# Optimization experiments

Hardware: AMD Instinct MI355X
Metric: run time of the kernel (lower is better)

## Reference

```python
import math
import jax, jax.numpy as jnp
import numpy as np

B, T, D = 4, 2048, 1024
H = 16
HD = D // H  # 64

def setup_inputs() -> dict:
    key = jax.random.key(0)
    k1, k2, k3 = jax.random.split(key, 3)
    x = jax.random.normal(k1, (B, T, D), dtype=jnp.float32)
    # weights stored as [in, out]; equivalent to torch Linear weight [out,in] transposed
    w_qkv = jax.random.normal(k2, (D, 3 * D), dtype=jnp.float32) * (1.0 / math.sqrt(D))
    w_out = jax.random.normal(k3, (D, D), dtype=jnp.float32) * (1.0 / math.sqrt(D))
    return {"x": x, "w_qkv": w_qkv, "w_out": w_out}

def reference(x, w_qkv, w_out):
    b, t, c = x.shape
    hd = c // H
    qkv = x @ w_qkv                                   # [B,T,3C]
    q, k, v = jnp.split(qkv, 3, axis=-1)
    # [B,T,C] -> [B,H,T,hd]
    q = q.reshape(b, t, H, hd).transpose(0, 2, 1, 3)
    k = k.reshape(b, t, H, hd).transpose(0, 2, 1, 3)
    v = v.reshape(b, t, H, hd).transpose(0, 2, 1, 3)
    scale = 1.0 / math.sqrt(hd)
    scores = jnp.einsum('bhqd,bhkd->bhqk', q, k) * scale  # [B,H,T,T]
    causal = jnp.tril(jnp.ones((t, t), dtype=bool))
    scores = jnp.where(causal, scores, jnp.finfo(scores.dtype).min)
    attn = jax.nn.softmax(scores, axis=-1)
    out = jnp.einsum('bhqk,bhkd->bhqd', attn, v)       # [B,H,T,hd]
    out = out.transpose(0, 2, 1, 3).reshape(b, t, c)
    return out @ w_out
```

## Files before the change

### kernel.cpp

```cpp
#include <hip/hip_runtime.h>
#include <stdint.h>
#include <stddef.h>

#define BB 4
#define TT 2048
#define DD 1024
#define HH 16
#define HDIM 64
#define BT (BB*TT)
#define N1 (3*DD)

typedef __attribute__((ext_vector_type(8))) short short8;
typedef __attribute__((ext_vector_type(4))) float floatx4;
typedef __attribute__((ext_vector_type(4))) unsigned short ushortx4;

__device__ __forceinline__ unsigned short f2b(float f) {
    unsigned int u = __float_as_uint(f);
    u += 0x7fffu + ((u >> 16) & 1u);
    return (unsigned short)(u >> 16);
}

__device__ __forceinline__ void gld_lds16(const void* g, void* l) {
    __builtin_amdgcn_global_load_lds(
        (__attribute__((address_space(1))) void*)(g),
        (__attribute__((address_space(3))) void*)(l), 16, 0, 0);
}

__global__ void cvt_bf16(const float* __restrict__ src, unsigned short* __restrict__ dst, int n4) {
    int i = blockIdx.x * blockDim.x + threadIdx.x;
    if (i < n4) {
        floatx4 f = ((const floatx4*)src)[i];
        ushortx4 o;
        o.x = f2b(f.x); o.y = f2b(f.y); o.z = f2b(f.z); o.w = f2b(f.w);
        ((ushortx4*)dst)[i] = o;
    }
}

__global__ void transpose_cvt(const float* __restrict__ src, unsigned short* __restrict__ dst,
                              int R, int C) {
    __shared__ float tile[32][33];
    const int c0 = blockIdx.x * 32, r0 = blockIdx.y * 32;
    const int x = threadIdx.x, y = threadIdx.y;
    for (int yy = y; yy < 32; yy += 8)
        tile[yy][x] = src[(size_t)(r0 + yy) * C + c0 + x];
    __syncthreads();
    for (int yy = y; yy < 32; yy += 8)
        dst[(size_t)(c0 + yy) * R + r0 + x] = f2b(tile[x][yy]);
}

template<int MODE>
__global__ __launch_bounds__(256, 3)
void gemm_bt(const unsigned short* __restrict__ A,
             const unsigned short* __restrict__ Bt,
             void* __restrict__ Cout, int M, int N, int K,
             float qscale, unsigned short* __restrict__ vt_out) {
    __shared__ unsigned short a_tile[2][128 * 32];
    __shared__ unsigned short b_tile[2][128 * 32];
    const int tid  = threadIdx.x;
    const int wave = tid >> 6;
    const int lane = tid & 63;
    const int quad = lane >> 4;
    const int lc   = lane & 15;
    const int wm = wave >> 1, wn = wave & 1;
    const int row0 = blockIdx.y * 128;
    const int col0 = blockIdx.x * 128;

    const int c0 = wave, c1 = wave + 4;
    const int r_in = lane >> 2;
    const int kseg = (lane & 3) * 8;
    const unsigned short* gA0 = A  + (size_t)(row0 + c0 * 16 + r_in) * K + kseg;
    const unsigned short* gA1 = A  + (size_t)(row0 + c1 * 16 + r_in) * K + kseg;
    const unsigned short* gB0 = Bt + (size_t)(col0 + c0 * 16 + r_in) * K + kseg;
    const unsigned short* gB1 = Bt + (size_t)(col0 + c1 * 16 + r_in) * K + kseg;
    const int sA0 = c0 * 512, sA1 = c1 * 512;

    floatx4 acc[4][4];
    #pragma unroll
    for (int i = 0; i < 4; i++)
        #pragma unroll
        for (int j = 0; j < 4; j++)
            acc[i][j] = (floatx4){0.f, 0.f, 0.f, 0.f};

    gld_lds16(gA0, &a_tile[0][sA0]);
    gld_lds16(gA1, &a_tile[0][sA1]);
    gld_lds16(gB0, &b_tile[0][sA0]);
    gld_lds16(gB1, &b_tile[0][sA1]);
    int buf = 0;

    const int nkt = K >> 5;
    for (int kt = 0; kt < nkt; ++kt) {
        __syncthreads();
        if (kt + 1 < nkt) {
            gA0 += 32; gA1 += 32; gB0 += 32; gB1 += 32;
            gld_lds16(gA0, &a_tile[buf ^ 1][sA0]);
            gld_lds16(gA1, &a_tile[buf ^ 1][sA1]);
            gld_lds16(gB0, &b_tile[buf ^ 1][sA0]);
            gld_lds16(gB1, &b_tile[buf ^ 1][sA1]);
        }

        short8 af[4], bf[4];
        #pragma unroll
        for (int mi = 0; mi < 4; ++mi)
            af[mi] = *(const short8*)&a_tile[buf][(wm * 64 + mi * 16 + lc) * 32 + quad * 8];
        #pragma unroll
        for (int ni = 0; ni < 4; ++ni)
            bf[ni] = *(const short8*)&b_tile[buf][(wn * 64 + ni * 16 + lc) * 32 + quad * 8];
        #pragma unroll
        for (int mi = 0; mi < 4; ++mi)
            #pragma unroll
            for (int ni = 0; ni < 4; ++ni)
                acc[mi][ni] = __builtin_amdgcn_mfma_f32_16x16x32_bf16(af[mi], bf[ni], acc[mi][ni], 0, 0, 0);
        buf ^= 1;
    }

    #pragma unroll
    for (int mi = 0; mi < 4; ++mi) {
        const int rbase = row0 + wm * 64 + mi * 16 + quad * 4;
        #pragma unroll
        for (int ni = 0; ni < 4; ++ni) {
            const int colbase = col0 + wn * 64 + ni * 16;
            const int col = colbase + lc;
            if (MODE == 0) {
                #pragma unroll
                for (int r = 0; r < 4; ++r)
                    ((float*)Cout)[(size_t)(rbase + r) * N + col] = acc[mi][ni][r];
            } else {
                if (colbase < 2 * DD) {
                    const float sc = (colbase < DD) ? qscale : 1.0f;
                    #pragma unroll
                    for (int r = 0; r < 4; ++r)
                        ((unsigned short*)Cout)[(size_t)(rbase + r) * N + col] = f2b(acc[mi][ni][r] * sc);
                } else {
                    const int vcol = col - 2 * DD;
                    const int hh = vcol >> 6, d = vcol & 63;
                    const int bq = rbase >> 11, t = rbase & 2047;
                    ushortx4 pk;
                    pk.x = f2b(acc[mi][ni][0]);
                    pk.y = f2b(acc[mi][ni][1]);
                    pk.z = f2b(acc[mi][ni][2]);
                    pk.w = f2b(acc[mi][ni][3]);
                    *(ushortx4*)&vt_out[(size_t)((bq * 16 + hh) * 64 + d) * TT + t] = pk;
                }
            }
        }
    }
}

__global__ __launch_bounds__(256, 2)
void attn_fwd(const unsigned short* __restrict__ qkv,
              const unsigned short* __restrict__ vt,
              unsigned short* __restrict__ out) {
    __shared__ unsigned short kbuf[2][64 * 64];
    __shared__ unsigned short vbuf[2][64 * 64];
    __shared__ unsigned short p_lds[4][32 * 72];
    const int bh = blockIdx.x;
    const int b = bh >> 4, h = bh & 15;
    const int pr = blockIdx.y;
    const int tid = threadIdx.x;
    const int wave = tid >> 6, lane = tid & 63;
    const int quad = lane >> 4, lc = lane & 15;
    unsigned short* pw = p_lds[wave];

    const int sr = wave * 8 + (lane >> 3);
    const int lg = (lane & 7) ^ (sr & 7);
    const unsigned short* ksrc0 = qkv + (size_t)(b * TT + sr) * N1 + DD + h * HDIM + lg * 8;
    const unsigned short* vsrc0 = vt + (size_t)(bh * HDIM + sr) * TT + lg * 8;
    const int stg = wave * 512;

    int fofs[4][2];
    #pragma unroll
    for (int mi = 0; mi < 4; ++mi)
        #pragma unroll
        for (int kk = 0; kk < 2; ++kk)
            fofs[mi][kk] = (mi * 16 + lc) * 64 + (((kk * 4 + quad) ^ (lc & 7)) * 8);

    gld_lds16(ksrc0, &kbuf[0][stg]);
    gld_lds16(ksrc0 + 32 * (size_t)N1, &kbuf[0][stg + 2048]);
    gld_lds16(vsrc0, &vbuf[0][stg]);
    gld_lds16(vsrc0 + 32 * (size_t)TT, &vbuf[0][stg + 2048]);
    int buf = 0;

    for (int pass = 0; pass < 2; ++pass) {
        const int j = pass ? (15 - pr) : pr;
        const int q0 = j * 128;
        const int r0 = q0 + wave * 32;
        const int tmax = 2 * j + 1;

        short8 qf[2][2];
        #pragma unroll
        for (int ni = 0; ni < 2; ++ni)
            #pragma unroll
            for (int kk = 0; kk < 2; ++kk)
                qf[ni][kk] = *(const short8*)(qkv + (size_t)(b * TT + r0 + ni * 16 + lc) * N1 + h * HDIM + kk * 32 + quad * 8);

        float lp[2] = {0.f, 0.f};
        floatx4 o_acc[4][2];
        #pragma unroll
        for (int mi = 0; mi < 4; ++mi)
            #pragma unroll
            for (int ni = 0; ni < 2; ++ni)
                o_acc[mi][ni] = (floatx4){0.f, 0.f, 0.f, 0.f};

        for (int t = 0; t <= tmax; ++t) {
            const int kv0 = t * 64;
            __syncthreads();

            const int nt = (t < tmax) ? (t + 1) : (pass == 0 ? 0 : -1);
            if (nt >= 0) {
                const unsigned short* ks = ksrc0 + (size_t)nt * 64 * N1;
                const unsigned short* vs = vsrc0 + nt * 64;
                gld_lds16(ks, &kbuf[buf ^ 1][stg]);
                gld_lds16(ks + 32 * (size_t)N1, &kbuf[buf ^ 1][stg + 2048]);
                gld_lds16(vs, &vbuf[buf ^ 1][stg]);
                gld_lds16(vs + 32 * (size_t)TT, &vbuf[buf ^ 1][stg + 2048]);
            }

            short8 kf[4][2];
            #pragma unroll
            for (int mi = 0; mi < 4; ++mi)
                #pragma unroll
                for (int kk = 0; kk < 2; ++kk)
                    kf[mi][kk] = *(const short8*)&kbuf[buf][fofs[mi][kk]];
            floatx4 sa[4][2];
            #pragma unroll
            for (int mi = 0; mi < 4; ++mi)
                #pragma unroll
                for (int ni = 0; ni < 2; ++ni) {
                    floatx4 z = (floatx4){0.f, 0.f, 0.f, 0.f};
                    z = __builtin_amdgcn_mfma_f32_16x16x32_bf16(kf[mi][0], qf[ni][0], z, 0, 0, 0);
                    z = __builtin_amdgcn_mfma_f32_16x16x32_bf16(kf[mi][1], qf[ni][1], z, 0, 0, 0);
                    sa[mi][ni] = z;
                }

            if (kv0 + 63 > r0) {
                #pragma unroll
                for (int ni = 0; ni < 2; ++ni) {
                    const int qg = r0 + ni * 16 + lc;
                    #pragma unroll
                    for (int mi = 0; mi < 4; ++mi) {
                        const int kvb = kv0 + mi * 16 + quad * 4;
                        #pragma unroll
                        for (int r = 0; r < 4; ++r)
                            sa[mi][ni][r] = (kvb + r <= qg) ? sa[mi][ni][r] : -1e30f;
                    }
                }
            }

            #pragma unroll
            for (int ni = 0; ni < 2; ++ni) {
                float rs = 0.f;
                #pragma unroll
                for (int mi = 0; mi < 4; ++mi) {
                    float p0 = __builtin_amdgcn_exp2f(sa[mi][ni][0]);
                    float p1 = __builtin_amdgcn_exp2f(sa[mi][ni][1]);
                    float p2 = __builtin_amdgcn_exp2f(sa[mi][ni][2]);
                    float p3 = __builtin_amdgcn_exp2f(sa[mi][ni][3]);
                    rs += (p0 + p1) + (p2 + p3);
                    ushortx4 pk;
                    pk.x = f2b(p0); pk.y = f2b(p1); pk.z = f2b(p2); pk.w = f2b(p3);
                    *(ushortx4*)&pw[(ni * 16 + lc) * 72 + mi * 16 + quad * 4] = pk;
                }
                lp[ni] += rs;
            }

            short8 pf[2][2];
            #pragma unroll
            for (int ni = 0; ni < 2; ++ni)
                #pragma unroll
                for (int kk = 0; kk < 2; ++kk)
                    pf[ni][kk] = *(const short8*)&pw[(ni * 16 + lc) * 72 + kk * 32 + quad * 8];
            short8 vf[4][2];
            #pragma unroll
            for (int mi = 0; mi < 4; ++mi)
                #pragma unroll
                for (int kk = 0; kk < 2; ++kk)
                    vf[mi][kk] = *(const short8*)&vbuf[buf][fofs[mi][kk]];
            #pragma unroll
            for (int mi = 0; mi < 4; ++mi)
                #pragma unroll
                for (int ni = 0; ni < 2; ++ni) {
                    o_acc[mi][ni] = __builtin_amdgcn_mfma_f32_16x16x32_bf16(vf[mi][0], pf[ni][0], o_acc[mi][ni], 0, 0, 0);
                    o_acc[mi][ni] = __builtin_amdgcn_mfma_f32_16x16x32_bf16(vf[mi][1], pf[ni][1], o_acc[mi][ni], 0, 0, 0);
                }

            buf ^= 1;
        }

        #pragma unroll
        for (int ni = 0; ni < 2; ++ni) {
            float lt = lp[ni];
            lt += __shfl_xor(lt, 16);
            lt += __shfl_xor(lt, 32);
            const float inv = 1.0f / lt;
            const size_t tok = (size_t)(b * TT + r0 + ni * 16 + lc);
            #pragma unroll
            for (int mi = 0; mi < 4; ++mi) {
                ushortx4 pk;
                pk.x = f2b(o_acc[mi][ni][0] * inv);
                pk.y = f2b(o_acc[mi][ni][1] * inv);
                pk.z = f2b(o_acc[mi][ni][2] * inv);
                pk.w = f2b(o_acc[mi][ni][3] * inv);
                *(ushortx4*)&out[tok * DD + h * HDIM + mi * 16 + quad * 4] = pk;
            }
        }
    }
}

extern "C" void kernel_launch(void* const* d_in, const int* in_sizes, int n_in,
                              void* d_out, int out_size, void* d_ws, size_t ws_size,
                              hipStream_t stream) {
    const float* x     = (const float*)d_in[0];
    const float* w_qkv = (const float*)d_in[1];
    const float* w_out = (const float*)d_in[2];
    float* out = (float*)d_out;

    unsigned short* ws  = (unsigned short*)d_ws;
    unsigned short* xb  = ws;
    unsigned short* qkv = xb  + (size_t)BT * DD;
    unsigned short* wqT = qkv + (size_t)BT * N1;
    unsigned short* woT = wqT + (size_t)N1 * DD;
    unsigned short* vtb = woT + (size_t)DD * DD;

    const float QSCALE = 0.18033688011112042f;

    cvt_bf16<<<(BT * DD / 4 + 255) / 256, 256, 0, stream>>>(x, xb, BT * DD / 4);
    transpose_cvt<<<dim3(N1 / 32, DD / 32), dim3(32, 8), 0, stream>>>(w_qkv, wqT, DD, N1);
    transpose_cvt<<<dim3(DD / 32, DD / 32), dim3(32, 8), 0, stream>>>(w_out, woT, DD, DD);
    gemm_bt<1><<<dim3(N1 / 128, BT / 128), 256, 0, stream>>>(xb, wqT, qkv, BT, N1, DD, QSCALE, vtb);
    attn_fwd<<<dim3(BB * HH, 8), 256, 0, stream>>>(qkv, vtb, xb);
    gemm_bt<0><<<dim3(DD / 128, BT / 128), 256, 0, stream>>>(xb, woT, out, BT, DD, DD, 1.0f, nullptr);
}
```

Baseline: 257.4 us.

## Use a larger 256x192 register tile for the QKV projection GEMM

Splits the templated GEMM into a dedicated QKV kernel using 256x192 block tiles with 8x6 MFMA accumulators per wave, and a simplified output-projection kernel. The larger tile raises data reuse per LDS load and cuts the block count, aiming to reduce memory traffic and load overhead in the QKV GEMM. It raises register pressure (192 accumulator registers per thread) and LDS usage, which may limit occupancy or cause spills.

```diff
diff --git a/kernel.cpp b/kernel.cpp
--- a/kernel.cpp
+++ b/kernel.cpp
@@ -48,12 +48,110 @@
         dst[(size_t)(c0 + yy) * R + r0 + x] = f2b(tile[x][yy]);
 }
 
-template<int MODE>
+__global__ __launch_bounds__(256, 2)
+void gemm_qkv(const unsigned short* __restrict__ A,
+              const unsigned short* __restrict__ Bt,
+              unsigned short* __restrict__ Cout, int M, int N, int K,
+              float qscale, unsigned short* __restrict__ vt_out) {
+    __shared__ unsigned short a_tile[2][256 * 32];
+    __shared__ unsigned short b_tile[2][192 * 32];
+    const int tid  = threadIdx.x;
+    const int wave = tid >> 6;
+    const int lane = tid & 63;
+    const int quad = lane >> 4;
+    const int lc   = lane & 15;
+    const int wm = wave >> 1, wn = wave & 1;
+    const int row0 = blockIdx.y * 256;
+    const int col0 = blockIdx.x * 192;
+
+    const int r_in = lane >> 2;
+    const int kseg = (lane & 3) * 8;
+    const unsigned short* gA0 = A  + (size_t)(row0 + (wave     ) * 16 + r_in) * K + kseg;
+    const unsigned short* gA1 = A  + (size_t)(row0 + (wave +  4) * 16 + r_in) * K + kseg;
+    const unsigned short* gA2 = A  + (size_t)(row0 + (wave +  8) * 16 + r_in) * K + kseg;
+    const unsigned short* gA3 = A  + (size_t)(row0 + (wave + 12) * 16 + r_in) * K + kseg;
+    const unsigned short* gB0 = Bt + (size_t)(col0 + (wave     ) * 16 + r_in) * K + kseg;
+    const unsigned short* gB1 = Bt + (size_t)(col0 + (wave +  4) * 16 + r_in) * K + kseg;
+    const unsigned short* gB2 = Bt + (size_t)(col0 + (wave +  8) * 16 + r_in) * K + kseg;
+    const int sA0 = (wave     ) * 512, sA1 = (wave +  4) * 512;
+    const int sA2 = (wave +  8) * 512, sA3 = (wave + 12) * 512;
+
+    floatx4 acc[8][6];
+    #pragma unroll
+    for (int i = 0; i < 8; i++)
+        #pragma unroll
+        for (int j = 0; j < 6; j++)
+            acc[i][j] = (floatx4){0.f, 0.f, 0.f, 0.f};
+
+    gld_lds16(gA0, &a_tile[0][sA0]);
+    gld_lds16(gA1, &a_tile[0][sA1]);
+    gld_lds16(gA2, &a_tile[0][sA2]);
+    gld_lds16(gA3, &a_tile[0][sA3]);
+    gld_lds16(gB0, &b_tile[0][sA0]);
+    gld_lds16(gB1, &b_tile[0][sA1]);
+    gld_lds16(gB2, &b_tile[0][sA2]);
+    int buf = 0;
+
+    const int nkt = K >> 5;
+    for (int kt = 0; kt < nkt; ++kt) {
+        __syncthreads();
+        if (kt + 1 < nkt) {
+            gA0 += 32; gA1 += 32; gA2 += 32; gA3 += 32;
+            gB0 += 32; gB1 += 32; gB2 += 32;
+            gld_lds16(gA0, &a_tile[buf ^ 1][sA0]);
+            gld_lds16(gA1, &a_tile[buf ^ 1][sA1]);
+            gld_lds16(gA2, &a_tile[buf ^ 1][sA2]);
+            gld_lds16(gA3, &a_tile[buf ^ 1][sA3]);
+            gld_lds16(gB0, &b_tile[buf ^ 1][sA0]);
+            gld_lds16(gB1, &b_tile[buf ^ 1][sA1]);
+            gld_lds16(gB2, &b_tile[buf ^ 1][sA2]);
+        }
+
+        short8 bf[6];
+        #pragma unroll
+        for (int ni = 0; ni < 6; ++ni)
+            bf[ni] = *(const short8*)&b_tile[buf][(wn * 96 + ni * 16 + lc) * 32 + quad * 8];
+        #pragma unroll
+        for (int mi = 0; mi < 8; ++mi) {
+            short8 af = *(const short8*)&a_tile[buf][(wm * 128 + mi * 16 + lc) * 32 + quad * 8];
+            #pragma unroll
+            for (int ni = 0; ni < 6; ++ni)
+                acc[mi][ni] = __builtin_amdgcn_mfma_f32_16x16x32_bf16(af, bf[ni], acc[mi][ni], 0, 0, 0);
+        }
+        buf ^= 1;
+    }
+
+    #pragma unroll
+    for (int mi = 0; mi < 8; ++mi) {
+        const int rbase = row0 + wm * 128 + mi * 16 + quad * 4;
+        #pragma unroll
+        for (int ni = 0; ni < 6; ++ni) {
+            const int colbase = col0 + wn * 96 + ni * 16;
+            const int col = colbase + lc;
+            if (colbase < 2 * DD) {
+                const float sc = (colbase < DD) ? qscale : 1.0f;
+                #pragma unroll
+                for (int r = 0; r < 4; ++r)
+                    Cout[(size_t)(rbase + r) * N + col] = f2b(acc[mi][ni][r] * sc);
+            } else {
+                const int vcol = col - 2 * DD;
+                const int hh = vcol >> 6, d = vcol & 63;
+                const int bq = rbase >> 11, t = rbase & 2047;
+                ushortx4 pk;
+                pk.x = f2b(acc[mi][ni][0]);
+                pk.y = f2b(acc[mi][ni][1]);
+                pk.z = f2b(acc[mi][ni][2]);
+                pk.w = f2b(acc[mi][ni][3]);
+                *(ushortx4*)&vt_out[(size_t)((bq * 16 + hh) * 64 + d) * TT + t] = pk;
+            }
+        }
+    }
+}
+
 __global__ __launch_bounds__(256, 3)
-void gemm_bt(const unsigned short* __restrict__ A,
-             const unsigned short* __restrict__ Bt,
-             void* __restrict__ Cout, int M, int N, int K,
-             float qscale, unsigned short* __restrict__ vt_out) {
+void gemm_out(const unsigned short* __restrict__ A,
+              const unsigned short* __restrict__ Bt,
+              float* __restrict__ Cout, int M, int N, int K) {
     __shared__ unsigned short a_tile[2][128 * 32];
     __shared__ unsigned short b_tile[2][128 * 32];
     const int tid  = threadIdx.x;
@@ -118,30 +216,10 @@
         const int rbase = row0 + wm * 64 + mi * 16 + quad * 4;
         #pragma unroll
         for (int ni = 0; ni < 4; ++ni) {
-            const int colbase = col0 + wn * 64 + ni * 16;
-            const int col = colbase + lc;
-            if (MODE == 0) {
-                #pragma unroll
-                for (int r = 0; r < 4; ++r)
-                    ((float*)Cout)[(size_t)(rbase + r) * N + col] = acc[mi][ni][r];
-            } else {
-                if (colbase < 2 * DD) {
-                    const float sc = (colbase < DD) ? qscale : 1.0f;
-                    #pragma unroll
-                    for (int r = 0; r < 4; ++r)
-                        ((unsigned short*)Cout)[(size_t)(rbase + r) * N + col] = f2b(acc[mi][ni][r] * sc);
-                } else {
-                    const int vcol = col - 2 * DD;
-                    const int hh = vcol >> 6, d = vcol & 63;
-                    const int bq = rbase >> 11, t = rbase & 2047;
-                    ushortx4 pk;
-                    pk.x = f2b(acc[mi][ni][0]);
-                    pk.y = f2b(acc[mi][ni][1]);
-                    pk.z = f2b(acc[mi][ni][2]);
-                    pk.w = f2b(acc[mi][ni][3]);
-                    *(ushortx4*)&vt_out[(size_t)((bq * 16 + hh) * 64 + d) * TT + t] = pk;
-                }
-            }
+            const int col = col0 + wn * 64 + ni * 16 + lc;
+            #pragma unroll
+            for (int r = 0; r < 4; ++r)
+                Cout[(size_t)(rbase + r) * N + col] = acc[mi][ni][r];
         }
     }
 }
@@ -326,7 +404,7 @@
     cvt_bf16<<<(BT * DD / 4 + 255) / 256, 256, 0, stream>>>(x, xb, BT * DD / 4);
     transpose_cvt<<<dim3(N1 / 32, DD / 32), dim3(32, 8), 0, stream>>>(w_qkv, wqT, DD, N1);
     transpose_cvt<<<dim3(DD / 32, DD / 32), dim3(32, 8), 0, stream>>>(w_out, woT, DD, DD);
-    gemm_bt<1><<<dim3(N1 / 128, BT / 128), 256, 0, stream>>>(xb, wqT, qkv, BT, N1, DD, QSCALE, vtb);
+    gemm_qkv<<<dim3(N1 / 192, BT / 256), 256, 0, stream>>>(xb, wqT, qkv, BT, N1, DD, QSCALE, vtb);
     attn_fwd<<<dim3(BB * HH, 8), 256, 0, stream>>>(qkv, vtb, xb);
-    gemm_bt<0><<<dim3(DD / 128, BT / 128), 256, 0, stream>>>(xb, woT, out, BT, DD, DD, 1.0f, nullptr);
-}
+    gemm_out<<<dim3(DD / 128, BT / 128), 256, 0, stream>>>(xb, woT, out, BT, DD, DD);
+}
```

New measurement: 245.7 us. -4.6%, faster.
